# Optimization experiments

Hardware: AMD Instinct MI355X
Metric: run time of the kernel (lower is better)

The kernel has to match this reference:

```python
import jax, jax.numpy as jnp
import numpy as np

B = 524288
D_IN = 128
D_OUT = 128
MASK_DENSITY = 0.25  # fraction of DAG edges present


def setup_inputs() -> dict:
    key = jax.random.key(0)
    k = jax.random.split(key, 6)
    x0 = jax.random.normal(k[0], (B, D_IN), dtype=jnp.float32)
    x1 = jax.random.normal(k[1], (B, D_IN), dtype=jnp.float32)
    # weights ~ N(0, 0.1^2) as in torch.normal(mean=0, std=0.1)
    w0 = jax.random.normal(k[2], (D_OUT, D_IN), dtype=jnp.float32) * 0.1
    w1 = jax.random.normal(k[3], (D_OUT, D_IN), dtype=jnp.float32) * 0.1
    # binary DAG connectivity masks [out_dim, in_dims[i]]
    m0 = (jax.random.uniform(k[4], (D_OUT, D_IN)) < MASK_DENSITY).astype(jnp.float32)
    m1 = (jax.random.uniform(k[5], (D_OUT, D_IN)) < MASK_DENSITY).astype(jnp.float32)
    return {"x0": x0, "x1": x1, "w0": w0, "w1": w1, "m0": m0, "m1": m1}


def reference(x0, x1, w0, w1, m0, m1):
    # sum_i  x_i @ (W_i * M_i)^T   -> [B, out_dim]
    # (note: original module creates self.bias but never adds it in forward)
    out = jnp.einsum("bi,oi->bo", x0, w0 * m0)
    out = out + jnp.einsum("bi,oi->bo", x1, w1 * m1)
    return out
```

## Files before the change

### kernel.cpp

```cpp
#include <hip/hip_runtime.h>

typedef __attribute__((ext_vector_type(8))) short bf16x8;
typedef __attribute__((ext_vector_type(4))) float f32x4;
typedef __attribute__((ext_vector_type(2))) unsigned int u32x2;

#define NBLK 512
#define NTHR 512
#define NT   16
#define DOUT 128

__device__ __forceinline__ unsigned short bf_rne(float x) {
  unsigned u = __builtin_bit_cast(unsigned, x);
  return (unsigned short)((u + 0x7FFFu + ((u >> 16) & 1u)) >> 16);
}
__device__ __forceinline__ void split2(float x, short& hi, short& lo) {
  unsigned u = __builtin_bit_cast(unsigned, x);
  float hf = __builtin_bit_cast(float, u & 0xFFFF0000u);
  hi = (short)(unsigned short)(u >> 16);
  lo = (short)bf_rne(x - hf);
}

__device__ __forceinline__ int fsw(int row) {
  return ((row & 7) << 2) | ((row >> 3) & 1);
}

__global__ __launch_bounds__(NTHR, 2)
void dagmm(const float* __restrict__ x0, const float* __restrict__ x1,
           const float* __restrict__ w0, const float* __restrict__ w1,
           const float* __restrict__ m0, const float* __restrict__ m1,
           float* __restrict__ out)
{
  __shared__ __align__(16) char L[131072];

  const int t_   = threadIdx.x;
  const int l    = t_ & 63;
  const int w    = t_ >> 6;
  const int l16  = l & 15;
  const int lq   = l >> 4;

  bf16x8 bhi[8], blo[8];
  {
    const int col = w * 16 + l16;
#pragma unroll
    for (int ks = 0; ks < 8; ++ks) {
      const int k0 = ks * 32 + lq * 8;
      const float* wp = (k0 < 128) ? (w0 + col * 128 + k0) : (w1 + col * 128 + (k0 - 128));
      const float* mp = (k0 < 128) ? (m0 + col * 128 + k0) : (m1 + col * 128 + (k0 - 128));
      float4 wa = *(const float4*)wp, wb = *(const float4*)(wp + 4);
      float4 ma = *(const float4*)mp, mb = *(const float4*)(mp + 4);
      float v[8] = {wa.x*ma.x, wa.y*ma.y, wa.z*ma.z, wa.w*ma.w,
                    wb.x*mb.x, wb.y*mb.y, wb.z*mb.z, wb.w*mb.w};
      bf16x8 hv, lv;
#pragma unroll
      for (int j = 0; j < 8; ++j) { short h, lo2; split2(v[j], h, lo2); hv[j] = h; lv[j] = lo2; }
      bhi[ks] = hv; blo[ks] = lv;
    }
  }

  const float* xb = (l < 32) ? (x0 + l * 4) : (x1 + (l - 32) * 4);
  const size_t Tbase = (size_t)blockIdx.x * NT * 64;

  float4 pf[8];

#define LOADREG(tt)                                                          \
  {                                                                          \
    _Pragma("unroll")                                                        \
    for (int s = 0; s < 8; ++s)                                              \
      pf[s] = *(const float4*)(xb + (Tbase + (size_t)(tt) * 64 + w * 8 + s) * 128); \
  }

#define SPLITWRITE(b)                                                        \
  {                                                                          \
    _Pragma("unroll")                                                        \
    for (int s = 0; s < 8; ++s) {                                            \
      const int row = w * 8 + s;                                             \
      short h0,h1,h2,h3, e0,e1,e2,e3;                                        \
      split2(pf[s].x, h0, e0); split2(pf[s].y, h1, e1);                      \
      split2(pf[s].z, h2, e2); split2(pf[s].w, h3, e3);                      \
      u32x2 hv, lv;                                                          \
      hv[0] = (unsigned short)h0 | ((unsigned)(unsigned short)h1 << 16);     \
      hv[1] = (unsigned short)h2 | ((unsigned)(unsigned short)h3 << 16);     \
      lv[0] = (unsigned short)e0 | ((unsigned)(unsigned short)e1 << 16);     \
      lv[1] = (unsigned short)e2 | ((unsigned)(unsigned short)e3 << 16);     \
      const int base = (b) * 65536 + row * 512 + (((l >> 1) ^ fsw(row)) << 4) + (l & 1) * 8; \
      *(u32x2*)(L + base)         = hv;                                      \
      *(u32x2*)(L + base + 32768) = lv;                                      \
    }                                                                        \
  }

  LOADREG(0);
  SPLITWRITE(0);
  LOADREG(1);
  asm volatile("s_waitcnt lgkmcnt(0)" ::: "memory");
  __builtin_amdgcn_s_barrier();
  asm volatile("" ::: "memory");

  for (int t = 0; t < NT; ++t) {
    if (t + 1 < NT) SPLITWRITE((t + 1) & 1);
    if (t + 2 < NT) LOADREG(t + 2);

    f32x4 acc[4];
#pragma unroll
    for (int rt = 0; rt < 4; ++rt) acc[rt] = (f32x4){0.f, 0.f, 0.f, 0.f};

    const int bb = (t & 1) * 65536;
#pragma unroll
    for (int ks = 0; ks < 8; ++ks) {
#pragma unroll
      for (int rt = 0; rt < 4; ++rt) {
        const int row = rt * 16 + l16;
        const int ba  = bb + row * 512 + (((ks * 4 + lq) ^ fsw(row)) << 4);
        bf16x8 xh = *(const bf16x8*)(L + ba);
        bf16x8 xl = *(const bf16x8*)(L + ba + 32768);
        acc[rt] = __builtin_amdgcn_mfma_f32_16x16x32_bf16(bhi[ks], xh, acc[rt], 0, 0, 0);
        acc[rt] = __builtin_amdgcn_mfma_f32_16x16x32_bf16(bhi[ks], xl, acc[rt], 0, 0, 0);
        acc[rt] = __builtin_amdgcn_mfma_f32_16x16x32_bf16(blo[ks], xh, acc[rt], 0, 0, 0);
      }
    }

#pragma unroll
    for (int rt = 0; rt < 4; ++rt) {
      const size_t row = Tbase + (size_t)t * 64 + rt * 16 + l16;
      *(f32x4*)&out[row * DOUT + w * 16 + lq * 4] = acc[rt];
    }

    asm volatile("s_waitcnt lgkmcnt(0)" ::: "memory");
    __builtin_amdgcn_s_barrier();
    asm volatile("" ::: "memory");
  }
}

extern "C" void kernel_launch(void* const* d_in, const int* in_sizes, int n_in,
                              void* d_out, int out_size, void* d_ws, size_t ws_size,
                              hipStream_t stream) {
  const float* x0 = (const float*)d_in[0];
  const float* x1 = (const float*)d_in[1];
  const float* w0 = (const float*)d_in[2];
  const float* w1 = (const float*)d_in[3];
  const float* m0 = (const float*)d_in[4];
  const float* m1 = (const float*)d_in[5];
  dagmm<<<NBLK, NTHR, 0, stream>>>(x0, x1, w0, w1, m0, m1, (float*)d_out);
}
```

Measured before the change: 178.2 us.

## Stage x tiles via global_load_lds and split into bf16 LDS fragments

Replaces register-staged global loads of x with direct global-to-LDS async loads (global_load_lds), then a separate pass reads the fp32 tile from LDS, splits it into bf16 hi/lo and writes MFMA-ready swizzled fragments. Tile height drops from 64 to 32 rows with twice as many iterations, using a double-buffered raw region and a double-buffered fragment region. The goal is to free VGPRs and overlap HBM loads with compute through vmcnt-based waits. The cost is an extra LDS round trip per tile and more barriers per row processed, and the hand-counted vmcnt values are fragile.

```diff
diff --git a/kernel.cpp b/kernel.cpp
--- a/kernel.cpp
+++ b/kernel.cpp
@@ -2,11 +2,10 @@
 
 typedef __attribute__((ext_vector_type(8))) short bf16x8;
 typedef __attribute__((ext_vector_type(4))) float f32x4;
-typedef __attribute__((ext_vector_type(2))) unsigned int u32x2;
 
 #define NBLK 512
 #define NTHR 512
-#define NT   16
+#define NT   32
 #define DOUT 128
 
 __device__ __forceinline__ unsigned short bf_rne(float x) {
@@ -20,8 +19,10 @@
   lo = (short)bf_rne(x - hf);
 }
 
-__device__ __forceinline__ int fsw(int row) {
-  return ((row & 7) << 2) | ((row >> 3) & 1);
+__device__ __forceinline__ void gll16(const float* g, char* l) {
+  __builtin_amdgcn_global_load_lds(
+      (const __attribute__((address_space(1))) unsigned int*)g,
+      (__attribute__((address_space(3))) unsigned int*)l, 16, 0, 0);
 }
 
 __global__ __launch_bounds__(NTHR, 2)
@@ -32,11 +33,11 @@
 {
   __shared__ __align__(16) char L[131072];
 
-  const int t_   = threadIdx.x;
-  const int l    = t_ & 63;
-  const int w    = t_ >> 6;
-  const int l16  = l & 15;
-  const int lq   = l >> 4;
+  const int t   = threadIdx.x;
+  const int l   = t & 63;
+  const int w   = t >> 6;
+  const int l16 = l & 15;
+  const int lq  = l >> 4;
 
   bf16x8 bhi[8], blo[8];
   {
@@ -57,61 +58,75 @@
     }
   }
 
-  const float* xb = (l < 32) ? (x0 + l * 4) : (x1 + (l - 32) * 4);
-  const size_t Tbase = (size_t)blockIdx.x * NT * 64;
+  const size_t Tbase = (size_t)blockIdx.x * (NT * 32);
 
-  float4 pf[8];
+  const float* xsrc = (l < 32) ? (x0 + l * 4) : (x1 + (l - 32) * 4);
 
-#define LOADREG(tt)                                                          \
-  {                                                                          \
-    _Pragma("unroll")                                                        \
-    for (int s = 0; s < 8; ++s)                                              \
-      pf[s] = *(const float4*)(xb + (Tbase + (size_t)(tt) * 64 + w * 8 + s) * 128); \
+#define ISSUE(ts, r)                                                        \
+  {                                                                         \
+    _Pragma("unroll")                                                       \
+    for (int i = 0; i < 4; ++i) {                                           \
+      const int row = w * 4 + i;                                            \
+      const size_t grow = Tbase + (size_t)(ts) * 32 + row;                  \
+      gll16(xsrc + grow * 128, L + (r) * 32768 + row * 1024);               \
+    }                                                                       \
   }
 
-#define SPLITWRITE(b)                                                        \
-  {                                                                          \
-    _Pragma("unroll")                                                        \
-    for (int s = 0; s < 8; ++s) {                                            \
-      const int row = w * 8 + s;                                             \
-      short h0,h1,h2,h3, e0,e1,e2,e3;                                        \
-      split2(pf[s].x, h0, e0); split2(pf[s].y, h1, e1);                      \
-      split2(pf[s].z, h2, e2); split2(pf[s].w, h3, e3);                      \
-      u32x2 hv, lv;                                                          \
-      hv[0] = (unsigned short)h0 | ((unsigned)(unsigned short)h1 << 16);     \
-      hv[1] = (unsigned short)h2 | ((unsigned)(unsigned short)h3 << 16);     \
-      lv[0] = (unsigned short)e0 | ((unsigned)(unsigned short)e1 << 16);     \
-      lv[1] = (unsigned short)e2 | ((unsigned)(unsigned short)e3 << 16);     \
-      const int base = (b) * 65536 + row * 512 + (((l >> 1) ^ fsw(row)) << 4) + (l & 1) * 8; \
-      *(u32x2*)(L + base)         = hv;                                      \
-      *(u32x2*)(L + base + 32768) = lv;                                      \
-    }                                                                        \
-  }
+  ISSUE(0, 0);
+  ISSUE(1, 1);
+  asm volatile("s_waitcnt vmcnt(4)" ::: "memory");
 
-  LOADREG(0);
-  SPLITWRITE(0);
-  LOADREG(1);
-  asm volatile("s_waitcnt lgkmcnt(0)" ::: "memory");
-  __builtin_amdgcn_s_barrier();
-  asm volatile("" ::: "memory");
+  const int rowS = w * 4 + (l >> 4);
+  const int kf   = (l & 15) * 16;
 
-  for (int t = 0; t < NT; ++t) {
-    if (t + 1 < NT) SPLITWRITE((t + 1) & 1);
-    if (t + 2 < NT) LOADREG(t + 2);
+  for (int tt = 0; tt < NT; ++tt) {
+    const int r = tt & 1;
 
-    f32x4 acc[4];
+    {
+      const char* Fb = L + r * 32768 + rowS * 1024 + kf * 4;
+      float4 v0 = ((const float4*)Fb)[0], v1 = ((const float4*)Fb)[1];
+      float4 v2 = ((const float4*)Fb)[2], v3 = ((const float4*)Fb)[3];
+      const int rt = rowS >> 4;
 #pragma unroll
-    for (int rt = 0; rt < 4; ++rt) acc[rt] = (f32x4){0.f, 0.f, 0.f, 0.f};
+      for (int q2 = 0; q2 < 2; ++q2) {
+        float vv[8];
+        if (q2 == 0) { vv[0]=v0.x; vv[1]=v0.y; vv[2]=v0.z; vv[3]=v0.w;
+                       vv[4]=v1.x; vv[5]=v1.y; vv[6]=v1.z; vv[7]=v1.w; }
+        else         { vv[0]=v2.x; vv[1]=v2.y; vv[2]=v2.z; vv[3]=v2.w;
+                       vv[4]=v3.x; vv[5]=v3.y; vv[6]=v3.z; vv[7]=v3.w; }
+        const int u  = (l & 15) * 2 + q2;
+        const int ks = u >> 2, kq = u & 3;
+        const int f  = rt * 8 + ks;
+        const int slot = (kq * 16 + (rowS & 15)) ^ ks;
+        bf16x8 hv, lv;
+#pragma unroll
+        for (int j = 0; j < 8; ++j) { short h, lo2; split2(vv[j], h, lo2); hv[j] = h; lv[j] = lo2; }
+        char* bp = L + 65536 + r * 32768 + f * 1024 + slot * 16;
+        *(bf16x8*)bp           = hv;
+        *(bf16x8*)(bp + 16384) = lv;
+      }
+    }
 
-    const int bb = (t & 1) * 65536;
+    asm volatile("s_waitcnt lgkmcnt(0)" ::: "memory");
+    __builtin_amdgcn_s_barrier();
+    asm volatile("" ::: "memory");
+
+    {
+      const int ts = (tt + 2 < NT) ? (tt + 2) : (NT - 1);
+      ISSUE(ts, r);
+    }
+    asm volatile("" ::: "memory");
+
+    f32x4 acc[2];
+    acc[0] = (f32x4){0.f, 0.f, 0.f, 0.f};
+    acc[1] = (f32x4){0.f, 0.f, 0.f, 0.f};
 #pragma unroll
     for (int ks = 0; ks < 8; ++ks) {
 #pragma unroll
-      for (int rt = 0; rt < 4; ++rt) {
-        const int row = rt * 16 + l16;
-        const int ba  = bb + row * 512 + (((ks * 4 + lq) ^ fsw(row)) << 4);
-        bf16x8 xh = *(const bf16x8*)(L + ba);
-        bf16x8 xl = *(const bf16x8*)(L + ba + 32768);
+      for (int rt = 0; rt < 2; ++rt) {
+        const char* bp = L + 65536 + r * 32768 + (rt * 8 + ks) * 1024 + ((l ^ ks) << 4);
+        bf16x8 xh = *(const bf16x8*)bp;
+        bf16x8 xl = *(const bf16x8*)(bp + 16384);
         acc[rt] = __builtin_amdgcn_mfma_f32_16x16x32_bf16(bhi[ks], xh, acc[rt], 0, 0, 0);
         acc[rt] = __builtin_amdgcn_mfma_f32_16x16x32_bf16(bhi[ks], xl, acc[rt], 0, 0, 0);
         acc[rt] = __builtin_amdgcn_mfma_f32_16x16x32_bf16(blo[ks], xh, acc[rt], 0, 0, 0);
@@ -119,15 +134,16 @@
     }
 
 #pragma unroll
-    for (int rt = 0; rt < 4; ++rt) {
-      const size_t row = Tbase + (size_t)t * 64 + rt * 16 + l16;
+    for (int rt = 0; rt < 2; ++rt) {
+      const size_t row = Tbase + (size_t)tt * 32 + rt * 16 + l16;
       *(f32x4*)&out[row * DOUT + w * 16 + lq * 4] = acc[rt];
     }
 
-    asm volatile("s_waitcnt lgkmcnt(0)" ::: "memory");
+    asm volatile("s_waitcnt vmcnt(6)" ::: "memory");
     __builtin_amdgcn_s_barrier();
     asm volatile("" ::: "memory");
   }
+#undef ISSUE
 }
 
 extern "C" void kernel_launch(void* const* d_in, const int* in_sizes, int n_in,
```

Measured after the change: 175.5 us. No clear change (-1.5%).
